# Optimization experiments

Hardware: AMD Instinct MI355X
Metric: run time of the kernel (lower is better)

Reference implementation:

```python
import jax, jax.numpy as jnp
import numpy as np

NS, NV = 16, 4          # scalar / vector multiplicities (model defaults)
N_NODES, N_EDGES = 50000, 400000
WEIGHT_NUMEL = NS * NS + NS * NV  # 320: paths 0e*0e->0e and 0e*1o->1o


def sph_harm_l012(vec):
    """Real spherical harmonics l=0,1,2 with e3nn 'component' normalization,
    evaluated on the normalized edge vectors. Output [E, 9]."""
    eps = 1e-8
    r = vec / (jnp.linalg.norm(vec, axis=-1, keepdims=True) + eps)
    x, y, z = r[:, 0], r[:, 1], r[:, 2]
    sh0 = jnp.ones_like(x)[:, None]
    c1 = np.float32(np.sqrt(3.0))
    sh1 = c1 * jnp.stack([x, y, z], -1)
    c2 = np.float32(np.sqrt(15.0))
    c2b = np.float32(np.sqrt(5.0) / 2.0)
    sh2 = jnp.stack([c2 * x * y, c2 * y * z, c2b * (3 * z * z - 1.0),
                     c2 * z * x, 0.5 * c2 * (x * x - y * y)], -1)
    return jnp.concatenate([sh0, sh1, sh2], -1)


def setup_inputs() -> dict:
    key = jax.random.key(0)
    ks = jax.random.split(key, 8)
    h = 3 * NS  # n_edge_features = hidden_features = 48
    node_attr = jax.random.normal(ks[0], (N_NODES, NS), jnp.float32)
    edge_attr = jax.random.normal(ks[1], (N_EDGES, h), jnp.float32)
    edge_vec = jax.random.normal(ks[2], (N_EDGES, 3), jnp.float32)
    edge_index = jax.random.randint(ks[3], (2, N_EDGES), 0, N_NODES)
    fc1_w = jax.random.normal(ks[4], (h, h), jnp.float32) / np.sqrt(h)
    fc1_b = jnp.zeros((h,), jnp.float32)
    fc2_w = jax.random.normal(ks[5], (h, WEIGHT_NUMEL), jnp.float32) / np.sqrt(h)
    fc2_b = jnp.zeros((WEIGHT_NUMEL,), jnp.float32)
    return {"node_attr": node_attr, "edge_attr": edge_attr, "edge_vec": edge_vec,
            "fc1_w": fc1_w, "fc1_b": fc1_b, "fc2_w": fc2_w, "fc2_b": fc2_b,
            "edge_index": edge_index}


def reference(node_attr, edge_attr, edge_vec, fc1_w, fc1_b, fc2_w, fc2_b, edge_index):
    N = node_attr.shape[0]
    E = edge_attr.shape[0]
    edge_src, edge_dst = edge_index[0], edge_index[1]

    # spherical harmonics of edge directions (build_*_conv_graph)
    edge_sh = sph_harm_l012(edge_vec)                 # [E, 9]

    # per-edge TP weights: fc = Linear -> ReLU -> Linear (dropout=0)
    w = jax.nn.relu(edge_attr @ fc1_w + fc1_b) @ fc2_w + fc2_b  # [E, 320]
    w0 = w[:, :NS * NS].reshape(E, NS, NS)            # path 0e x 0e -> 0e
    w1 = w[:, NS * NS:].reshape(E, NS, NV)            # path 0e x 1o -> 1o

    # gather destination-node features
    x = node_attr[edge_dst]                           # [E, NS]

    # FullyConnectedTensorProduct('16x0e', sh, '16x0e + 4x1o'):
    # fan-in per output = NS (mul_u * mul_v summed over paths) -> 1/sqrt(NS)
    inv = np.float32(1.0 / np.sqrt(NS))
    out0 = jnp.einsum('euw,eu->ew', w0, x) * edge_sh[:, :1] * inv       # [E, NS]
    out1 = jnp.einsum('euw,eu,em->ewm', w1, x, edge_sh[:, 1:4]) * inv   # [E, NV, 3]
    msg = jnp.concatenate([out0, out1.reshape(E, NV * 3)], -1)          # [E, NS+3*NV]

    # scatter-mean over edge_src (reduce='mean', dim_size=N)
    summed = jax.ops.segment_sum(msg, edge_src, num_segments=N)
    cnt = jax.ops.segment_sum(jnp.ones((E,), msg.dtype), edge_src, num_segments=N)
    return summed / jnp.maximum(cnt, 1.0)[:, None]
```

## Files before the change

### kernel.cpp

```cpp
#include <hip/hip_runtime.h>
#include <hip/hip_bf16.h>
#include <math.h>

#define NS 16
#define H  48
#define TB 256
#define THREADS 512

typedef __attribute__((ext_vector_type(8))) short bf16x8;
typedef __attribute__((ext_vector_type(4))) float f32x4;

#define W2O   2304
#define B1H   20224
#define ZO    20272
#define ATO   20280
#define XO_   36664
#define SMEM_HW 40760
#define MSGF  10140
#define WCPY  2535

__device__ __forceinline__ short f2bf(float f) {
    unsigned b = __float_as_uint(f);
    unsigned r = (b + 0x7FFFu + ((b >> 16) & 1u)) >> 16;
    return (short)r;
}
__device__ __forceinline__ float bf2f(short s) {
    return __uint_as_float(((unsigned)(unsigned short)s) << 16);
}
__device__ __forceinline__ unsigned cvtpk(float lo, float hi) {
    unsigned r;
    asm("v_cvt_pk_bf16_f32 %0, %1, %2" : "=v"(r) : "v"(lo), "v"(hi));
    return r;
}
__device__ __forceinline__ uint4 pk8(float4 a, float4 b) {
    uint4 q;
    q.x = cvtpk(a.x, a.y); q.y = cvtpk(a.z, a.w);
    q.z = cvtpk(b.x, b.y); q.w = cvtpk(b.z, b.w);
    return q;
}

__global__ __launch_bounds__(256) void prep_hist_kernel(
    const float* __restrict__ fc1_w, const float* __restrict__ fc2_w,
    const float* __restrict__ fc1_b, const float* __restrict__ fc2_b,
    short* __restrict__ wpack,
    const int* __restrict__ edge_index, int* __restrict__ deg, int E)
{
    if (blockIdx.x < 6) {
        int t = blockIdx.x * 256 + threadIdx.x;
        if (t < 1472) {
            int f = t >> 6, l = t & 63;
            bool isW1 = (f < 3);
            int u = isW1 ? f : (f - 3);
            int n = u * 16 + (l & 15);
            const float* W = isW1 ? fc1_w : fc2_w;
            int ldw = isW1 ? 48 : 320;
            int base = isW1 ? (f * 768) : (W2O + u * 896);
            short* d0 = wpack + base + l * 8;
            #pragma unroll
            for (int i = 0; i < 8; ++i)
                d0[i] = f2bf(W[((l >> 4) * 8 + i) * ldw + n]);
            if (l < 32) {
                short* d1 = wpack + base + 512 + l * 8;
                #pragma unroll
                for (int i = 0; i < 8; ++i)
                    d1[i] = f2bf(W[(32 + (l >> 4) * 8 + i) * ldw + n]);
            } else if (!isW1 && l < 48) {
                short* d1 = wpack + base + 512 + l * 8;
                d1[0] = f2bf(fc2_b[n]);
                #pragma unroll
                for (int i = 1; i < 8; ++i) d1[i] = 0;
            }
        } else if (t < 1520) {
            wpack[B1H + (t - 1472)] = f2bf(fc1_b[t - 1472]);
        } else if (t < 1528) {
            wpack[ZO + (t - 1520)] = 0;
        }
    } else {
        int i = (blockIdx.x - 6) * 256 + threadIdx.x;
        if (i < E) atomicAdd(deg + edge_index[i], 1);
    }
}

__global__ __launch_bounds__(THREADS, 2) void edge_mfma_kernel(
    const float* __restrict__ node_attr,
    const float* __restrict__ edge_attr,
    const float* __restrict__ edge_vec,
    const short* __restrict__ wpack,
    const int*   __restrict__ edge_index,
    unsigned short* __restrict__ msg,
    int*   __restrict__ cursor,
    int E)
{
    __shared__ __align__(16) short smemS[SMEM_HW];
    float* smemF = (float*)smemS;
    const int tid = threadIdx.x;
    const int base = blockIdx.x * TB;
    const int l  = tid & 63;
    const int wv = tid >> 6;
    const int g  = l >> 4;
    const int c  = l & 15;
    const int rb = wv * 32;

    const int r = tid >> 1, h = tid & 1;
    const int e = base + r;
    const int ce = e < E ? e : (E - 1);
    const int sI_raw = edge_index[ce];
    const int dI = edge_index[E + ce];

    float shx_r = 0.f, shy_r = 0.f, shz_r = 0.f;
    int slot_r = 0;

    for (int idx = tid; idx < WCPY; idx += THREADS) {
        uint4 v = ((const uint4*)wpack)[idx];
        *(uint4*)&smemS[idx * 8] = v;
    }

    {
        const float* ap = edge_attr + (size_t)ce * H + h * 24;
        float4 A0 = *(const float4*)(ap + 0);
        float4 A1 = *(const float4*)(ap + 4);
        float4 A2 = *(const float4*)(ap + 8);
        float4 A3 = *(const float4*)(ap + 12);
        float4 A4 = *(const float4*)(ap + 16);
        float4 A5 = *(const float4*)(ap + 20);
        const float* xp = node_attr + (size_t)dI * NS + h * 8;
        float4 X0 = *(const float4*)(xp + 0);
        float4 X1 = *(const float4*)(xp + 4);
        if (e >= E) {
            A0 = make_float4(0,0,0,0); A1 = A0; A2 = A0; A3 = A0; A4 = A0; A5 = A0;
            X0 = A0; X1 = A0;
        }
        const int s8 = (r & 7) << 3;
        *(uint4*)&smemS[ATO + r * 64 + (((h*3 + 0) << 3) ^ s8)] = pk8(A0, A1);
        *(uint4*)&smemS[ATO + r * 64 + (((h*3 + 1) << 3) ^ s8)] = pk8(A2, A3);
        *(uint4*)&smemS[ATO + r * 64 + (((h*3 + 2) << 3) ^ s8)] = pk8(A4, A5);
        {
            int az = ATO + r * 64 + (((6 + h) << 3) ^ s8);
            uint4 zq;
            zq.x = (h == 0) ? 0x00003F80u : 0u;
            zq.y = 0u; zq.z = 0u; zq.w = 0u;
            *(uint4*)&smemS[az] = zq;
        }
        *(uint4*)&smemS[XO_ + r * 16 + h * 8] = pk8(X0, X1);
        if (h == 0) {
            int sI = (e < E) ? sI_raw : 0;
            float vx = 0.f, vy = 0.f, vz = 0.f;
            if (e < E) {
                vx = edge_vec[3 * (size_t)ce + 0];
                vy = edge_vec[3 * (size_t)ce + 1];
                vz = edge_vec[3 * (size_t)ce + 2];
            }
            float rn = 1.0f / (sqrtf(vx*vx + vy*vy + vz*vz) + 1e-8f);
            const float c1 = 1.7320508075688772f;
            shx_r = c1 * vx * rn; shy_r = c1 * vy * rn; shz_r = c1 * vz * rn;
            if (e < E) slot_r = atomicAdd(cursor + sI, 1);
        }
    }
    __syncthreads();

    bf16x8 a0[2], a1[2];
    #pragma unroll
    for (int m = 0; m < 2; ++m) {
        int row = rb + m * 16 + c, s8 = (row & 7) << 3;
        a0[m] = *(const bf16x8*)&smemS[ATO + row * 64 + ((g * 8) ^ s8)];
        a1[m] = *(const bf16x8*)&smemS[ATO + row * 64 + ((32 + g * 8) ^ s8)];
    }
    #pragma unroll
    for (int fr = 0; fr < 3; ++fr) {
        bf16x8 b0 = *(const bf16x8*)&smemS[fr * 768 + l * 8];
        bf16x8 b1 = *(const bf16x8*)&smemS[(l < 32) ? (fr * 768 + 512 + l * 8) : ZO];
        float bia = bf2f(smemS[B1H + fr * 16 + c]);
        #pragma unroll
        for (int m = 0; m < 2; ++m) {
            f32x4 acc = {0.f, 0.f, 0.f, 0.f};
            acc = __builtin_amdgcn_mfma_f32_16x16x32_bf16(a0[m], b0, acc, 0, 0, 0);
            acc = __builtin_amdgcn_mfma_f32_16x16x32_bf16(a1[m], b1, acc, 0, 0, 0);
            float t0 = fmaxf(acc[0] + bia, 0.f);
            float t1 = fmaxf(acc[1] + bia, 0.f);
            float t2 = fmaxf(acc[2] + bia, 0.f);
            float t3 = fmaxf(acc[3] + bia, 0.f);
            unsigned p01 = cvtpk(t0, t1);
            unsigned p23 = cvtpk(t2, t3);
            int row0 = rb + m * 16 + g * 4;
            int col = fr * 16 + c;
            smemS[ATO + (row0+0) * 64 + (col ^ (((row0+0) & 7) << 3))] = (short)p01;
            smemS[ATO + (row0+1) * 64 + (col ^ (((row0+1) & 7) << 3))] = (short)(p01 >> 16);
            smemS[ATO + (row0+2) * 64 + (col ^ (((row0+2) & 7) << 3))] = (short)p23;
            smemS[ATO + (row0+3) * 64 + (col ^ (((row0+3) & 7) << 3))] = (short)(p23 >> 16);
        }
    }

    bf16x8 tf0[2], tf1[2];
    #pragma unroll
    for (int m = 0; m < 2; ++m) {
        int row = rb + m * 16 + c, s8 = (row & 7) << 3;
        tf0[m] = *(const bf16x8*)&smemS[ATO + row * 64 + ((g * 8) ^ s8)];
        tf1[m] = *(const bf16x8*)&smemS[ATO + row * 64 + ((32 + g * 8) ^ s8)];
    }
    bf16x8 xr0[2][4], xr1[2][4];
    #pragma unroll
    for (int m = 0; m < 2; ++m)
        #pragma unroll
        for (int j = 0; j < 4; ++j) {
            int row = rb + m * 16 + g * 4 + j;
            xr0[m][j] = *(const bf16x8*)&smemS[XO_ + row * 16];
            xr1[m][j] = *(const bf16x8*)&smemS[XO_ + row * 16 + 8];
        }

    float o0[2][4] = {{0.f,0.f,0.f,0.f},{0.f,0.f,0.f,0.f}};
    float o1[2][4] = {{0.f,0.f,0.f,0.f},{0.f,0.f,0.f,0.f}};
    const int s2 = c >> 2;
    #pragma unroll
    for (int u = 0; u < 20; ++u) {
        const int wb = W2O + u * 896;
        bf16x8 b0 = *(const bf16x8*)&smemS[wb + l * 8];
        bf16x8 b1 = *(const bf16x8*)&smemS[(l < 48) ? (wb + 512 + l * 8) : ZO];
        #pragma unroll
        for (int m = 0; m < 2; ++m) {
            f32x4 acc = {0.f, 0.f, 0.f, 0.f};
            acc = __builtin_amdgcn_mfma_f32_16x16x32_bf16(tf0[m], b0, acc, 0, 0, 0);
            acc = __builtin_amdgcn_mfma_f32_16x16x32_bf16(tf1[m], b1, acc, 0, 0, 0);
            if (u < 16) {
                #pragma unroll
                for (int j = 0; j < 4; ++j) {
                    float xu = bf2f(u < 8 ? xr0[m][j][u] : xr1[m][j][u - 8]);
                    o0[m][j] = fmaf(xu, acc[j], o0[m][j]);
                }
            } else {
                const int f = u - 16;
                #pragma unroll
                for (int j = 0; j < 4; ++j) {
                    float e0, e1, e2, e3;
                    if (f < 2) {
                        e0 = bf2f(xr0[m][j][f*4+0]); e1 = bf2f(xr0[m][j][f*4+1]);
                        e2 = bf2f(xr0[m][j][f*4+2]); e3 = bf2f(xr0[m][j][f*4+3]);
                    } else {
                        e0 = bf2f(xr1[m][j][(f-2)*4+0]); e1 = bf2f(xr1[m][j][(f-2)*4+1]);
                        e2 = bf2f(xr1[m][j][(f-2)*4+2]); e3 = bf2f(xr1[m][j][(f-2)*4+3]);
                    }
                    float xu = e0;
                    xu = (s2 == 1) ? e1 : xu;
                    xu = (s2 == 2) ? e2 : xu;
                    xu = (s2 == 3) ? e3 : xu;
                    o1[m][j] = fmaf(xu, acc[j], o1[m][j]);
                }
            }
        }
    }
    #pragma unroll
    for (int m = 0; m < 2; ++m)
        #pragma unroll
        for (int j = 0; j < 4; ++j) {
            o1[m][j] += __shfl_xor(o1[m][j], 4);
            o1[m][j] += __shfl_xor(o1[m][j], 8);
        }

    const float inv = 0.25f;
    #pragma unroll
    for (int m = 0; m < 2; ++m)
        #pragma unroll
        for (int j = 0; j < 4; ++j) {
            const int rloc = m*16 + g*4 + j;
            const int rr = rb + rloc;
            const int srcl = rloc * 2;
            float shx = __shfl(shx_r, srcl);
            float shy = __shfl(shy_r, srcl);
            float shz = __shfl(shz_r, srcl);
            int lsrc = (g << 4) + (c < 12 ? c / 3 : 0);
            float ov = __shfl(o1[m][j], lsrc);
            int m3 = c - 3 * (c / 3);
            float shm = (m3 == 0) ? shx : ((m3 == 1) ? shy : shz);
            float v2 = (c < 12) ? ov * shm * inv : 0.f;
            smemF[MSGF + rr * 32 + c]      = o0[m][j] * inv;
            smemF[MSGF + rr * 32 + 16 + c] = v2;
        }

    #pragma unroll
    for (int it = 0; it < 4; ++it) {
        int rloc2 = it * 8 + (l >> 3);
        int r2 = rb + rloc2;
        int ch = (l & 7) * 4;
        int e2 = base + r2;
        int slot = __shfl(slot_r, rloc2 * 2);
        float4 val = *(const float4*)&smemF[MSGF + r2 * 32 + ch];
        if (e2 < E) {
            uint2 pv;
            pv.x = cvtpk(val.x, val.y);
            pv.y = cvtpk(val.z, val.w);
            *(uint2*)(msg + (size_t)slot * 32 + ch) = pv;
        }
    }
}

__global__ __launch_bounds__(1024) void offsets_kernel(
    const int* __restrict__ deg, int* __restrict__ starts,
    int* __restrict__ cursor, int* __restrict__ gtotal, int N)
{
    __shared__ int lds[1024];
    __shared__ int base_s;
    const int t = threadIdx.x;
    const int i = blockIdx.x * 1024 + t;
    int v = (i < N) ? deg[i] : 0;
    lds[t] = v;
    __syncthreads();
    int acc = v;
    for (int off = 1; off < 1024; off <<= 1) {
        int u = (t >= off) ? lds[t - off] : 0;
        __syncthreads();
        acc += u;
        lds[t] = acc;
        __syncthreads();
    }
    if (t == 1023) base_s = atomicAdd(gtotal, acc);
    __syncthreads();
    int excl = acc - v;
    if (i < N) {
        int s = base_s + excl;
        starts[i] = s;
        cursor[i] = s;
    }
}

__global__ __launch_bounds__(256) void sum_kernel(
    const unsigned short* __restrict__ msg, const int* __restrict__ starts,
    const int* __restrict__ deg, float* __restrict__ out, int N)
{
    int n = (blockIdx.x * blockDim.x + threadIdx.x) >> 5;
    int ch = threadIdx.x & 31;
    if (n >= N) return;
    int s = starts[n], d = deg[n];
    const unsigned short* mb = msg + (size_t)s * 32 + ch;
    float a0 = 0.f, a1 = 0.f, a2 = 0.f, a3 = 0.f;
    int k = 0;
    for (; k + 4 <= d; k += 4) {
        a0 += bf2f((short)mb[(size_t)(k + 0) * 32]);
        a1 += bf2f((short)mb[(size_t)(k + 1) * 32]);
        a2 += bf2f((short)mb[(size_t)(k + 2) * 32]);
        a3 += bf2f((short)mb[(size_t)(k + 3) * 32]);
    }
    if (k + 2 <= d) {
        a0 += bf2f((short)mb[(size_t)(k + 0) * 32]);
        a1 += bf2f((short)mb[(size_t)(k + 1) * 32]);
        k += 2;
    }
    if (k < d) a2 += bf2f((short)mb[(size_t)k * 32]);
    float acc = (a0 + a1) + (a2 + a3);
    if (ch < 28) out[(size_t)n * 28 + ch] = acc / fmaxf((float)d, 1.0f);
}

__global__ __launch_bounds__(256) void finalize_kernel(
    float* __restrict__ out, const float* __restrict__ cnt, int total)
{
    int i = blockIdx.x * blockDim.x + threadIdx.x;
    if (i < total) {
        float cv = cnt[i / 28];
        out[i] = out[i] / fmaxf(cv, 1.0f);
    }
}

__global__ __launch_bounds__(256) void naive_kernel(
    const float* __restrict__ node_attr, const float* __restrict__ edge_attr,
    const float* __restrict__ edge_vec, const float* __restrict__ fc1_w,
    const float* __restrict__ fc1_b, const float* __restrict__ fc2_w,
    const float* __restrict__ fc2_b, const int* __restrict__ edge_index,
    float* __restrict__ out, float* __restrict__ cnt, int E)
{
    int e = blockIdx.x * blockDim.x + threadIdx.x;
    if (e >= E) return;
    float a[H];
    for (int i = 0; i < H; ++i) a[i] = edge_attr[(size_t)e*H + i];
    int dst = edge_index[E + e];
    float x[NS];
    for (int i = 0; i < NS; ++i) x[i] = node_attr[(size_t)dst*NS + i];
    float o0[NS] = {0}, o1v[4] = {0};
    for (int k = 0; k < H; ++k) {
        float tk = fc1_b[k];
        for (int j = 0; j < H; ++j) tk = fmaf(a[j], fc1_w[j*H + k], tk);
        tk = fmaxf(tk, 0.f);
        const float* row = fc2_w + k*320;
        for (int u = 0; u < NS; ++u) {
            float q = tk * x[u];
            for (int w = 0; w < NS; ++w) o0[w] = fmaf(q, row[u*NS+w], o0[w]);
            for (int v = 0; v < 4; ++v) o1v[v] = fmaf(q, row[256+u*4+v], o1v[v]);
        }
    }
    for (int u = 0; u < NS; ++u) {
        float xu = x[u];
        for (int w = 0; w < NS; ++w) o0[w] = fmaf(xu, fc2_b[u*NS+w], o0[w]);
        for (int v = 0; v < 4; ++v) o1v[v] = fmaf(xu, fc2_b[256+u*4+v], o1v[v]);
    }
    float vx = edge_vec[3*(size_t)e], vy = edge_vec[3*(size_t)e+1], vz = edge_vec[3*(size_t)e+2];
    float rn = 1.0f / (sqrtf(vx*vx+vy*vy+vz*vz) + 1e-8f);
    const float c1 = 1.7320508075688772f;
    float sx = c1*vx*rn, sy = c1*vy*rn, sz = c1*vz*rn;
    int src = edge_index[e];
    float* ob = out + (size_t)src * 28;
    for (int w = 0; w < NS; ++w) atomicAdd(ob + w, o0[w] * 0.25f);
    for (int v = 0; v < 4; ++v) {
        float q = o1v[v] * 0.25f;
        atomicAdd(ob + 16 + 3*v + 0, q * sx);
        atomicAdd(ob + 16 + 3*v + 1, q * sy);
        atomicAdd(ob + 16 + 3*v + 2, q * sz);
    }
    atomicAdd(cnt + src, 1.0f);
}

extern "C" void kernel_launch(void* const* d_in, const int* in_sizes, int n_in,
                              void* d_out, int out_size, void* d_ws, size_t ws_size,
                              hipStream_t stream) {
    const float* node_attr  = (const float*)d_in[0];
    const float* edge_attr  = (const float*)d_in[1];
    const float* edge_vec   = (const float*)d_in[2];
    const float* fc1_w      = (const float*)d_in[3];
    const float* fc1_b      = (const float*)d_in[4];
    const float* fc2_w      = (const float*)d_in[5];
    const float* fc2_b      = (const float*)d_in[6];
    const int*   edge_index = (const int*)d_in[7];

    int E = in_sizes[2] / 3;
    int N = in_sizes[0] / NS;
    float* out = (float*)d_out;

    size_t msg_b  = (size_t)E * 32 * sizeof(unsigned short);
    size_t ints_b = (3 * (size_t)N + 1) * sizeof(int);
    size_t wpk_b  = (size_t)WCPY * 16;
    size_t need   = msg_b + ints_b + wpk_b;

    if (ws_size >= need) {
        unsigned short* msg = (unsigned short*)d_ws;
        int* ip     = (int*)((char*)d_ws + msg_b);
        int* deg    = ip;
        int* gtotal = ip + N;
        int* starts = ip + N + 1;
        int* cursor = ip + 2 * N + 1;
        short* wpack = (short*)((char*)d_ws + msg_b + ints_b);

        hipMemsetAsync(deg, 0, ((size_t)N + 1) * sizeof(int), stream);
        int nhist = (E + 255) / 256;
        prep_hist_kernel<<<6 + nhist, 256, 0, stream>>>(
            fc1_w, fc2_w, fc1_b, fc2_b, wpack, edge_index, deg, E);
        offsets_kernel<<<(N + 1023) / 1024, 1024, 0, stream>>>(
            deg, starts, cursor, gtotal, N);
        edge_mfma_kernel<<<(E + TB - 1) / TB, THREADS, 0, stream>>>(
            node_attr, edge_attr, edge_vec, wpack, edge_index, msg, cursor, E);
        sum_kernel<<<((size_t)N * 32 + 255) / 256, 256, 0, stream>>>(
            msg, starts, deg, out, N);
    } else {
        float* cnt = (float*)d_ws;
        hipMemsetAsync(d_out, 0, (size_t)out_size * sizeof(float), stream);
        hipMemsetAsync(d_ws, 0, (size_t)N * sizeof(float), stream);
        naive_kernel<<<(E + 255) / 256, 256, 0, stream>>>(
            node_attr, edge_attr, edge_vec, fc1_w, fc1_b, fc2_w, fc2_b,
            edge_index, out, cnt, E);
        int total = N * 28;
        finalize_kernel<<<(total + 255) / 256, 256, 0, stream>>>(out, cnt, total);
    }
}
```

Before: 101.0 us.

## Fuse memset, weight pack, histogram and offset scan into one cooperative kernel

```diff
diff --git a/kernel.cpp b/kernel.cpp
--- a/kernel.cpp
+++ b/kernel.cpp
@@ -1,6 +1,9 @@
 #include <hip/hip_runtime.h>
 #include <hip/hip_bf16.h>
+#include <hip/hip_cooperative_groups.h>
 #include <math.h>
+
+namespace cg = cooperative_groups;
 
 #define NS 16
 #define H  48
@@ -39,14 +42,24 @@
     return q;
 }
 
-__global__ __launch_bounds__(256) void prep_hist_kernel(
+__global__ __launch_bounds__(1024) void setup_kernel(
     const float* __restrict__ fc1_w, const float* __restrict__ fc2_w,
     const float* __restrict__ fc1_b, const float* __restrict__ fc2_b,
     short* __restrict__ wpack,
-    const int* __restrict__ edge_index, int* __restrict__ deg, int E)
+    const int* __restrict__ edge_index,
+    int* __restrict__ deg, int* __restrict__ starts,
+    int* __restrict__ cursor, int* __restrict__ gtotal,
+    int N, int E)
 {
-    if (blockIdx.x < 6) {
-        int t = blockIdx.x * 256 + threadIdx.x;
+    cg::grid_group grid = cg::this_grid();
+    const int gt = blockIdx.x * 1024 + threadIdx.x;
+    const int gs = gridDim.x * 1024;
+
+    for (int i = gt; i < N; i += gs) deg[i] = 0;
+    if (gt == 0) *gtotal = 0;
+    grid.sync();
+
+    for (int t = gt; t < 1528; t += gs) {
         if (t < 1472) {
             int f = t >> 6, l = t & 63;
             bool isW1 = (f < 3);
@@ -72,12 +85,35 @@
             }
         } else if (t < 1520) {
             wpack[B1H + (t - 1472)] = f2bf(fc1_b[t - 1472]);
-        } else if (t < 1528) {
+        } else {
             wpack[ZO + (t - 1520)] = 0;
         }
-    } else {
-        int i = (blockIdx.x - 6) * 256 + threadIdx.x;
-        if (i < E) atomicAdd(deg + edge_index[i], 1);
+    }
+    for (int i = gt; i < E; i += gs) atomicAdd(deg + edge_index[i], 1);
+    grid.sync();
+
+    __shared__ int lds[1024];
+    __shared__ int base_s;
+    const int t = threadIdx.x;
+    const int i = blockIdx.x * 1024 + t;
+    int v = (i < N) ? deg[i] : 0;
+    lds[t] = v;
+    __syncthreads();
+    int acc = v;
+    for (int off = 1; off < 1024; off <<= 1) {
+        int u = (t >= off) ? lds[t - off] : 0;
+        __syncthreads();
+        acc += u;
+        lds[t] = acc;
+        __syncthreads();
+    }
+    if (t == 1023) base_s = atomicAdd(gtotal, acc);
+    __syncthreads();
+    int excl = acc - v;
+    if (i < N) {
+        int s = base_s + excl;
+        starts[i] = s;
+        cursor[i] = s;
     }
 }
 
@@ -292,60 +328,37 @@
     }
 }
 
-__global__ __launch_bounds__(1024) void offsets_kernel(
-    const int* __restrict__ deg, int* __restrict__ starts,
-    int* __restrict__ cursor, int* __restrict__ gtotal, int N)
-{
-    __shared__ int lds[1024];
-    __shared__ int base_s;
-    const int t = threadIdx.x;
-    const int i = blockIdx.x * 1024 + t;
-    int v = (i < N) ? deg[i] : 0;
-    lds[t] = v;
-    __syncthreads();
-    int acc = v;
-    for (int off = 1; off < 1024; off <<= 1) {
-        int u = (t >= off) ? lds[t - off] : 0;
-        __syncthreads();
-        acc += u;
-        lds[t] = acc;
-        __syncthreads();
-    }
-    if (t == 1023) base_s = atomicAdd(gtotal, acc);
-    __syncthreads();
-    int excl = acc - v;
-    if (i < N) {
-        int s = base_s + excl;
-        starts[i] = s;
-        cursor[i] = s;
-    }
-}
-
 __global__ __launch_bounds__(256) void sum_kernel(
     const unsigned short* __restrict__ msg, const int* __restrict__ starts,
     const int* __restrict__ deg, float* __restrict__ out, int N)
 {
     int n = (blockIdx.x * blockDim.x + threadIdx.x) >> 5;
-    int ch = threadIdx.x & 31;
+    int hl = threadIdx.x & 31;
     if (n >= N) return;
     int s = starts[n], d = deg[n];
-    const unsigned short* mb = msg + (size_t)s * 32 + ch;
-    float a0 = 0.f, a1 = 0.f, a2 = 0.f, a3 = 0.f;
-    int k = 0;
-    for (; k + 4 <= d; k += 4) {
-        a0 += bf2f((short)mb[(size_t)(k + 0) * 32]);
-        a1 += bf2f((short)mb[(size_t)(k + 1) * 32]);
-        a2 += bf2f((short)mb[(size_t)(k + 2) * 32]);
-        a3 += bf2f((short)mb[(size_t)(k + 3) * 32]);
-    }
-    if (k + 2 <= d) {
-        a0 += bf2f((short)mb[(size_t)(k + 0) * 32]);
-        a1 += bf2f((short)mb[(size_t)(k + 1) * 32]);
-        k += 2;
-    }
-    if (k < d) a2 += bf2f((short)mb[(size_t)k * 32]);
-    float acc = (a0 + a1) + (a2 + a3);
-    if (ch < 28) out[(size_t)n * 28 + ch] = acc / fmaxf((float)d, 1.0f);
+    const int kg = hl >> 4;
+    const int cp = hl & 15;
+    const unsigned short* mb = msg + (size_t)s * 32 + cp * 2;
+    float alo0 = 0.f, ahi0 = 0.f, alo1 = 0.f, ahi1 = 0.f;
+    int k = kg;
+    for (; k + 2 < d; k += 4) {
+        unsigned v0 = *(const unsigned*)(mb + (size_t)k * 32);
+        unsigned v1 = *(const unsigned*)(mb + (size_t)(k + 2) * 32);
+        alo0 += bf2f((short)(v0 & 0xffff)); ahi0 += bf2f((short)(v0 >> 16));
+        alo1 += bf2f((short)(v1 & 0xffff)); ahi1 += bf2f((short)(v1 >> 16));
+    }
+    if (k < d) {
+        unsigned v0 = *(const unsigned*)(mb + (size_t)k * 32);
+        alo0 += bf2f((short)(v0 & 0xffff)); ahi0 += bf2f((short)(v0 >> 16));
+    }
+    float alo = alo0 + alo1, ahi = ahi0 + ahi1;
+    alo += __shfl_xor(alo, 16);
+    ahi += __shfl_xor(ahi, 16);
+    if (kg == 0 && cp < 14) {
+        float dn = 1.0f / fmaxf((float)d, 1.0f);
+        float2 o; o.x = alo * dn; o.y = ahi * dn;
+        *(float2*)(out + (size_t)n * 28 + cp * 2) = o;
+    }
 }
 
 __global__ __launch_bounds__(256) void finalize_kernel(
@@ -435,12 +448,13 @@
         int* cursor = ip + 2 * N + 1;
         short* wpack = (short*)((char*)d_ws + msg_b + ints_b);
 
-        hipMemsetAsync(deg, 0, ((size_t)N + 1) * sizeof(int), stream);
-        int nhist = (E + 255) / 256;
-        prep_hist_kernel<<<6 + nhist, 256, 0, stream>>>(
-            fc1_w, fc2_w, fc1_b, fc2_b, wpack, edge_index, deg, E);
-        offsets_kernel<<<(N + 1023) / 1024, 1024, 0, stream>>>(
-            deg, starts, cursor, gtotal, N);
+        int nb = (N + 1023) / 1024;
+        void* args[] = { (void*)&fc1_w, (void*)&fc2_w, (void*)&fc1_b,
+                         (void*)&fc2_b, (void*)&wpack, (void*)&edge_index,
+                         (void*)&deg, (void*)&starts, (void*)&cursor,
+                         (void*)&gtotal, (void*)&N, (void*)&E };
+        hipLaunchCooperativeKernel((void*)setup_kernel, dim3(nb), dim3(1024),
+                                   args, 0, stream);
         edge_mfma_kernel<<<(E + TB - 1) / TB, THREADS, 0, stream>>>(
             node_attr, edge_attr, edge_vec, wpack, edge_index, msg, cursor, E);
         sum_kernel<<<((size_t)N * 32 + 255) / 256, 256, 0, stream>>>(
```

Result: slower. 129.9 us (+28.7%).
